# Optimization experiments

Hardware: AMD Instinct MI355X
Metric: run time of the kernel (lower is better)

Reference implementation:

```python
import jax, jax.numpy as jnp
import numpy as np

N = 1_000_000
B = 4096
L = 4
CC = 3
K = (L + 1) ** 2  # 25


def setup_inputs() -> dict:
    key = jax.random.key(0)
    ks = jax.random.split(key, 20)
    points = jax.random.normal(ks[0], (N, 3), dtype=jnp.float32)
    color = jax.random.uniform(ks[1], (N, 3), dtype=jnp.float32)
    batch = jnp.sort(jax.random.randint(ks[2], (N,), 0, B, dtype=jnp.int64))

    def lin(k, o, i, s):
        return jax.random.normal(k, (o, i), dtype=jnp.float32) * s

    inp = {
        "points": points,
        "color": color,
        "batch": batch,
        # FeatureNet 1x1 conv weights (kernel size 1 -> plain linear)
        "w1": lin(ks[3], 32, 6, 0.4), "b1": jnp.zeros((32,), jnp.float32),
        "w2": lin(ks[4], 128, 32, 0.18), "b2": jnp.zeros((128,), jnp.float32),
        "w3": lin(ks[5], 256, 128, 0.09), "b3": jnp.zeros((256,), jnp.float32),
        # FC head
        "fw1": lin(ks[6], 128, 256, 0.06), "fb1": jnp.zeros((128,), jnp.float32),
        "fw2": lin(ks[7], 64, 128, 0.09), "fb2": jnp.zeros((64,), jnp.float32),
        "fw3": lin(ks[8], K * CC, 64, 0.12), "fb3": jnp.zeros((K * CC,), jnp.float32),
        "coef_mean": jnp.zeros((K, CC), jnp.float32),
        "coef_std": jnp.ones((K, CC), jnp.float32),
    }
    return inp


def reference(points, color, batch, w1, b1, w2, b2, w3, b3,
              fw1, fb1, fw2, fb2, fw3, fb3, coef_mean, coef_std):
    # per-point shared MLP (1x1 convs == linear over channel dim)
    x = jnp.concatenate([points, color], axis=-1)          # [N, 6]
    x = jax.nn.relu(x @ w1.T + b1)                          # [N, 32]
    x = jax.nn.relu(x @ w2.T + b2)                          # [N, 128]
    x = x @ w3.T + b3                                       # [N, 256]
    # scatter_reduce(amax) onto a zeros-initialized target (include_self=True)
    # => per-segment max clamped below at 0; empty segments stay 0.
    seg = jax.ops.segment_max(x, batch, num_segments=B, indices_are_sorted=True)
    x_max = jnp.maximum(seg, 0.0)                           # [B, 256]
    # FC head
    h = jax.nn.relu(x_max @ fw1.T + fb1)                    # [B, 128]
    h = jax.nn.relu(h @ fw2.T + fb2)                        # [B, 64]
    h = h @ fw3.T + fb3                                     # [B, 75]
    out = h.reshape(-1, K, CC) * coef_std + coef_mean       # [B, 25, 3]
    return out
```

## Files before the change

kernel.cpp:

```cpp
#include <hip/hip_runtime.h>
#include <hip/hip_bf16.h>

typedef __attribute__((ext_vector_type(8))) short short8;
typedef __attribute__((ext_vector_type(16))) float f32x16;

union U8 { short8 s; unsigned int u[4]; };

static __device__ __forceinline__ unsigned short f2bf(float f) {
  unsigned int u = __float_as_uint(f);
  u += 0x7fffu + ((u >> 16) & 1u);
  return (unsigned short)(u >> 16);
}
static __device__ __forceinline__ float bf2f(unsigned short h) {
  return __uint_as_float(((unsigned int)h) << 16);
}
static __device__ __forceinline__ unsigned int cvtpk(float lo, float hi) {
  unsigned int r;
  asm("v_cvt_pk_bf16_f32 %0, %1, %2" : "=v"(r) : "v"(lo), "v"(hi));
  return r;
}
static __device__ __forceinline__ unsigned int pkrelu(float a, float b) {
  return cvtpk(fmaxf(a, 0.0f), fmaxf(b, 0.0f));
}
static __device__ __forceinline__ f32x16 MFMA(short8 a, short8 b, f32x16 c) {
  return __builtin_amdgcn_mfma_f32_32x32x16_bf16(a, b, c, 0, 0, 0);
}

__global__ void prep_weights(const float* __restrict__ w1, const float* __restrict__ w2,
                             const float* __restrict__ w3,
                             unsigned short* __restrict__ w1p, uint4* __restrict__ wimg) {
  const int i = blockIdx.x * 256 + threadIdx.x;
  if (i < 512) {
    { int c = i >> 4, k = i & 15; w1p[i] = (k < 6) ? f2bf(w1[c * 6 + k]) : (unsigned short)0; }
    const int l31 = i & 31, rest = i >> 5;
    const int g = rest & 1, n = (rest >> 1) & 1, t2 = rest >> 2;
    const float* src = w2 + (l31 + 32 * t2) * 32 + n * 16 + 8 * g;
    uint4 v;
    v.x = (unsigned)f2bf(src[0]) | ((unsigned)f2bf(src[1]) << 16);
    v.y = (unsigned)f2bf(src[2]) | ((unsigned)f2bf(src[3]) << 16);
    v.z = (unsigned)f2bf(src[4]) | ((unsigned)f2bf(src[5]) << 16);
    v.w = (unsigned)f2bf(src[6]) | ((unsigned)f2bf(src[7]) << 16);
    wimg[i] = v;
  }
  if (i < 4096) {
    const int l31 = i & 31, rest = i >> 5;
    const int g = rest & 1, k0 = (rest >> 1) & 7, t = rest >> 4;
    const float* src = w3 + (l31 + 32 * t) * 128 + k0 * 16 + 8 * g;
    uint4 v;
    v.x = (unsigned)f2bf(src[0]) | ((unsigned)f2bf(src[1]) << 16);
    v.y = (unsigned)f2bf(src[2]) | ((unsigned)f2bf(src[3]) << 16);
    v.z = (unsigned)f2bf(src[4]) | ((unsigned)f2bf(src[5]) << 16);
    v.w = (unsigned)f2bf(src[6]) | ((unsigned)f2bf(src[7]) << 16);
    wimg[512 + i] = v;
  }
}

__global__ void seg_starts(const int* __restrict__ batch, int* __restrict__ starts,
                           int N, int B) {
  const int i = blockIdx.x * 256 + threadIdx.x;
  if (i == 0) {
    const int b0 = batch[0];
    for (int s = 0; s <= b0; ++s) starts[s] = 0;
    const int bl = batch[N - 1];
    for (int s = bl + 1; s <= B; ++s) starts[s] = N;
  } else if (i < N) {
    const int a = batch[i - 1], b = batch[i];
    for (int s = a + 1; s <= b; ++s) starts[s] = i;
  }
}

__global__ __launch_bounds__(512, 4) void mlp_segmax_mfma(
    const float* __restrict__ points, const float* __restrict__ color,
    const int* __restrict__ batch,
    const unsigned short* __restrict__ w1p, const uint4* __restrict__ wimg,
    const float* __restrict__ b1, const float* __restrict__ b2, const float* __restrict__ b3,
    float* __restrict__ xmax, int* __restrict__ Pid, unsigned short* __restrict__ Pval,
    int useP, int N)
{
  __shared__ __align__(16) uint4 smem[4608];
  const int tid  = threadIdx.x;
  const int wv   = tid >> 6;
  const int lane = tid & 63;
  const int g    = lane >> 5;
  const int l31  = lane & 31;

  for (int i = tid; i < 4608; i += 512) smem[i] = wimg[i];
  __syncthreads();
  const char* w2c = (const char*)smem;
  const char* w3c = (const char*)(smem + 512);

  const short8 a1 = *reinterpret_cast<const short8*>(w1p + l31 * 16 + 8 * g);
  float b3v[8];
#pragma unroll
  for (int t = 0; t < 8; ++t) b3v[t] = b3[32 * t + l31];

  const int wid = blockIdx.x * 8 + wv;
  const long long wbase = (long long)wid * 256;
  const int rowbase = 4 * wid;
  int rowcnt = 0;
  int cur = -1;
  float rmax[8];
#pragma unroll
  for (int t = 0; t < 8; ++t) rmax[t] = -INFINITY;

  auto flushP = [&]() {
    if (cur < 0) return;
    if (useP && rowcnt < 4) {
      const int row = rowbase + rowcnt;
      ++rowcnt;
      if (lane == 0) Pid[row] = cur;
#pragma unroll
      for (int t = 0; t < 8; ++t) {
        float v = fmaxf(rmax[t], __shfl_xor(rmax[t], 32));
        if ((t >> 2) == g) Pval[row * 256 + 32 * t + l31] = f2bf(v);
      }
    } else {
#pragma unroll
      for (int t = 0; t < 8; ++t) {
        float v = fmaxf(rmax[t], __shfl_xor(rmax[t], 32));
        if (lane < 32 && v > 0.0f)
          atomicMax((int*)xmax + cur * 256 + 32 * t + lane, __float_as_int(v));
      }
    }
  };

  float n0 = 0, n1 = 0, n2 = 0, n3 = 0, n4 = 0, n5 = 0;
  int nseg = -2 - lane;
  if (wbase < (long long)N) {
    const int p = (int)wbase + l31;
    n0 = points[p * 3 + 0]; n1 = points[p * 3 + 1]; n2 = points[p * 3 + 2];
    n3 = color[p * 3 + 0];  n4 = color[p * 3 + 1];  n5 = color[p * 3 + 2];
    nseg = batch[p];
  }

  for (int it = 0; it < 8; ++it) {
    const long long base = wbase + (long long)it * 32;
    if (base >= (long long)N) break;

    const float c0 = n0, c1 = n1, c2 = n2, c3 = n3, c4 = n4, c5 = n5;
    const int segv = nseg;
    if (base + 32 < (long long)N && it < 7) {
      const int p = (int)base + 32 + l31;
      n0 = points[p * 3 + 0]; n1 = points[p * 3 + 1]; n2 = points[p * 3 + 2];
      n3 = color[p * 3 + 0];  n4 = color[p * 3 + 1];  n5 = color[p * 3 + 2];
      nseg = batch[p];
    }

    unsigned long long b1a = (unsigned long long)b1; asm volatile("" : "+s"(b1a));
    unsigned long long b2a = (unsigned long long)b2; asm volatile("" : "+s"(b2a));
    const float* b1l = (const float*)b1a;
    const float* b2l = (const float*)b2a;
    int z = 0; asm volatile("" : "+v"(z));

    const unsigned int zm = (g == 0) ? 0xffffffffu : 0u;
    U8 bin;
    bin.u[0] = cvtpk(c0, c1) & zm;
    bin.u[1] = cvtpk(c2, c3) & zm;
    bin.u[2] = cvtpk(c4, c5) & zm;
    bin.u[3] = 0;
    f32x16 ci;
#pragma unroll
    for (int q2 = 0; q2 < 4; ++q2) {
      const float4 bv = *reinterpret_cast<const float4*>(b1l + 8 * q2 + 4 * g);
      ci[4 * q2 + 0] = bv.x; ci[4 * q2 + 1] = bv.y; ci[4 * q2 + 2] = bv.z; ci[4 * q2 + 3] = bv.w;
    }
    f32x16 d1 = MFMA(a1, bin.s, ci);

    unsigned int W1[4][2];
#pragma unroll
    for (int q2 = 0; q2 < 4; ++q2) {
      W1[q2][0] = pkrelu(d1[4 * q2 + 0], d1[4 * q2 + 1]);
      W1[q2][1] = pkrelu(d1[4 * q2 + 2], d1[4 * q2 + 3]);
    }
    U8 h1f[2];
#pragma unroll
    for (int n = 0; n < 2; ++n) {
      unsigned int r0 = __shfl_xor(W1[2 * n + 1 - g][0], 32);
      unsigned int r1 = __shfl_xor(W1[2 * n + 1 - g][1], 32);
      h1f[n].u[0] = (g == 0) ? W1[2 * n + g][0] : r0;
      h1f[n].u[1] = (g == 0) ? W1[2 * n + g][1] : r1;
      h1f[n].u[2] = (g == 1) ? W1[2 * n + g][0] : r0;
      h1f[n].u[3] = (g == 1) ? W1[2 * n + g][1] : r1;
    }

    unsigned int own2[4][2][2], rc2[4][2][2];
#pragma unroll
    for (int t2 = 0; t2 < 4; ++t2) {
      f32x16 cc;
#pragma unroll
      for (int q2 = 0; q2 < 4; ++q2) {
        const float4 bv = *reinterpret_cast<const float4*>(b2l + 32 * t2 + 8 * q2 + 4 * g);
        cc[4 * q2 + 0] = bv.x; cc[4 * q2 + 1] = bv.y; cc[4 * q2 + 2] = bv.z; cc[4 * q2 + 3] = bv.w;
      }
      const short8 a20 = *reinterpret_cast<const short8*>(
          w2c + ((((t2 * 2 + 0) * 2 + g) * 32 + l31) << 4) + z);
      const short8 a21 = *reinterpret_cast<const short8*>(
          w2c + ((((t2 * 2 + 1) * 2 + g) * 32 + l31) << 4) + z);
      f32x16 d2 = MFMA(a20, h1f[0].s, cc);
      d2 = MFMA(a21, h1f[1].s, d2);
      unsigned int Wt[4][2];
#pragma unroll
      for (int q2 = 0; q2 < 4; ++q2) {
        Wt[q2][0] = pkrelu(d2[4 * q2 + 0], d2[4 * q2 + 1]);
        Wt[q2][1] = pkrelu(d2[4 * q2 + 2], d2[4 * q2 + 3]);
      }
#pragma unroll
      for (int m = 0; m < 2; ++m) {
        own2[t2][m][0] = Wt[2 * m + g][0];
        own2[t2][m][1] = Wt[2 * m + g][1];
        rc2[t2][m][0] = __shfl_xor(Wt[2 * m + 1 - g][0], 32);
        rc2[t2][m][1] = __shfl_xor(Wt[2 * m + 1 - g][1], 32);
      }
    }
    U8 a3[8];
#pragma unroll
    for (int k0 = 0; k0 < 8; ++k0) {
      const int t2 = k0 >> 1, m = k0 & 1;
      a3[k0].u[0] = (g == 0) ? own2[t2][m][0] : rc2[t2][m][0];
      a3[k0].u[1] = (g == 0) ? own2[t2][m][1] : rc2[t2][m][1];
      a3[k0].u[2] = (g == 1) ? own2[t2][m][0] : rc2[t2][m][0];
      a3[k0].u[3] = (g == 1) ? own2[t2][m][1] : rc2[t2][m][1];
    }

    const int segA = __builtin_amdgcn_readfirstlane(segv);
    const int segD = __shfl(segv, 31);
    const bool caseU = (segA == segD);
    if (segA != cur) {
      flushP();
#pragma unroll
      for (int t = 0; t < 8; ++t) rmax[t] = -INFINITY;
      cur = segA;
    }
    unsigned int bA = 0, bD = 0;
    bool restAny = false;
    int rowA = -1;
    if (!caseU) {
      bA = (unsigned int)__ballot(segv == segA);
      bD = (unsigned int)__ballot(segv == segD);
      restAny = ((bA | bD) != 0xffffffffu);
      if (useP && rowcnt < 4) {
        rowA = rowbase + rowcnt;
        ++rowcnt;
        if (lane == 0) Pid[rowA] = segA;
      }
    }

#pragma unroll
    for (int t = 0; t < 8; ++t) {
      f32x16 acc;
#pragma unroll
      for (int r2 = 0; r2 < 16; ++r2) acc[r2] = b3v[t];
#pragma unroll
      for (int k0 = 0; k0 < 8; ++k0) {
        const short8 bf = *reinterpret_cast<const short8*>(
            w3c + ((((t * 8 + k0) * 2 + g) * 32 + l31) << 4) + z);
        acc = MFMA(a3[k0].s, bf, acc);
      }
      if (caseU) {
        float m = acc[0];
#pragma unroll
        for (int r2 = 1; r2 < 16; ++r2) m = fmaxf(m, acc[r2]);
        rmax[t] = fmaxf(rmax[t], m);
      } else {
        float ma = -INFINITY, md = -INFINITY;
#pragma unroll
        for (int r2 = 0; r2 < 16; ++r2) {
          const int idx = (r2 & 3) + 8 * (r2 >> 2) + 4 * g;
          const unsigned int bit = 1u << idx;
          const float v = acc[r2];
          ma = fmaxf(ma, (bA & bit) ? v : -INFINITY);
          md = fmaxf(md, (bD & bit) ? v : -INFINITY);
        }
        if (restAny) {
#pragma unroll
          for (int r2 = 0; r2 < 16; ++r2) {
            const int idx = (r2 & 3) + 8 * (r2 >> 2) + 4 * g;
            const unsigned int bit = 1u << idx;
            if (!((bA | bD) & bit)) {
              const int sid = __shfl(segv, idx);
              const float v = acc[r2];
              if (sid >= 0 && v > 0.0f)
                atomicMax((int*)xmax + sid * 256 + 32 * t + l31, __float_as_int(v));
            }
          }
        }
        float va = fmaxf(rmax[t], ma);
        va = fmaxf(va, __shfl_xor(va, 32));
        if (rowA >= 0) {
          if ((t >> 2) == g) Pval[rowA * 256 + 32 * t + l31] = f2bf(va);
        } else if (lane < 32 && va > 0.0f) {
          atomicMax((int*)xmax + segA * 256 + 32 * t + lane, __float_as_int(va));
        }
        rmax[t] = md;
      }
    }
    if (!caseU) cur = segD;
  }
  flushP();
  if (useP && lane == 0) {
    for (int j = rowcnt; j < 4; ++j) Pid[rowbase + j] = -1;
  }
}

__global__ __launch_bounds__(256) void head_kernel(
    const float* __restrict__ xmax,
    const int* __restrict__ starts, const int* __restrict__ Pid,
    const unsigned short* __restrict__ Pval, int useP,
    const float* __restrict__ fw1, const float* __restrict__ fb1,
    const float* __restrict__ fw2, const float* __restrict__ fb2,
    const float* __restrict__ fw3, const float* __restrict__ fb3,
    const float* __restrict__ cmean, const float* __restrict__ cstd,
    float* __restrict__ out, int B)
{
  __shared__ __align__(16) float xm[16][260];
  __shared__ __align__(16) float h1b[16][132];
  __shared__ __align__(16) float h2b[16][68];

  const int t = threadIdx.x;
  const int bbase = blockIdx.x * 16;

  for (int i = t; i < 16 * 256; i += 256) {
    const int bi = i >> 8, k = i & 255;
    const int s = min(bbase + bi, B - 1);
    float acc = xmax[(long long)s * 256 + k];
    if (useP) {
      const int i0 = starts[s], i1 = starts[s + 1];
      if (i1 > i0) {
        const int w0 = i0 >> 8, w1 = (i1 - 1) >> 8;
        for (int w = w0; w <= w1; ++w) {
#pragma unroll
          for (int j = 0; j < 4; ++j) {
            const int row = 4 * w + j;
            if (Pid[row] == s) acc = fmaxf(acc, bf2f(Pval[row * 256 + k]));
          }
        }
      }
    }
    xm[bi][k] = fmaxf(acc, 0.0f);
  }
  __syncthreads();

  {
    const int bi = t >> 4, oi = t & 15;
    float acc[8];
#pragma unroll
    for (int u = 0; u < 8; ++u) acc[u] = fb1[oi * 8 + u];
    for (int k = 0; k < 256; k += 4) {
      const float4 xv = *reinterpret_cast<const float4*>(&xm[bi][k]);
#pragma unroll
      for (int u = 0; u < 8; ++u) {
        const float4 wv = *reinterpret_cast<const float4*>(fw1 + (oi * 8 + u) * 256 + k);
        acc[u] = fmaf(xv.x, wv.x, acc[u]);
        acc[u] = fmaf(xv.y, wv.y, acc[u]);
        acc[u] = fmaf(xv.z, wv.z, acc[u]);
        acc[u] = fmaf(xv.w, wv.w, acc[u]);
      }
    }
#pragma unroll
    for (int u = 0; u < 8; ++u) h1b[bi][oi * 8 + u] = fmaxf(acc[u], 0.0f);
  }
  __syncthreads();

  {
    const int bi = t >> 4, oi = t & 15;
    float acc[4];
#pragma unroll
    for (int u = 0; u < 4; ++u) acc[u] = fb2[oi * 4 + u];
    for (int k = 0; k < 128; k += 4) {
      const float4 xv = *reinterpret_cast<const float4*>(&h1b[bi][k]);
#pragma unroll
      for (int u = 0; u < 4; ++u) {
        const float4 wv = *reinterpret_cast<const float4*>(fw2 + (oi * 4 + u) * 128 + k);
        acc[u] = fmaf(xv.x, wv.x, acc[u]);
        acc[u] = fmaf(xv.y, wv.y, acc[u]);
        acc[u] = fmaf(xv.z, wv.z, acc[u]);
        acc[u] = fmaf(xv.w, wv.w, acc[u]);
      }
    }
#pragma unroll
    for (int u = 0; u < 4; ++u) h2b[bi][oi * 4 + u] = fmaxf(acc[u], 0.0f);
  }
  __syncthreads();

  for (int i = t; i < 16 * 75; i += 256) {
    const int bi = i / 75, o = i - bi * 75;
    float a = fb3[o];
    for (int k = 0; k < 64; k += 4) {
      const float4 xv = *reinterpret_cast<const float4*>(&h2b[bi][k]);
      const float4 wv = *reinterpret_cast<const float4*>(fw3 + o * 64 + k);
      a = fmaf(xv.x, wv.x, a);
      a = fmaf(xv.y, wv.y, a);
      a = fmaf(xv.z, wv.z, a);
      a = fmaf(xv.w, wv.w, a);
    }
    const int b = bbase + bi;
    if (b < B) out[(long long)b * 75 + o] = fmaf(a, cstd[o], cmean[o]);
  }
}

extern "C" void kernel_launch(void* const* d_in, const int* in_sizes, int n_in,
                              void* d_out, int out_size, void* d_ws, size_t ws_size,
                              hipStream_t stream) {
  const float* points = (const float*)d_in[0];
  const float* color  = (const float*)d_in[1];
  const int*   batch  = (const int*)d_in[2];
  const float* w1  = (const float*)d_in[3];
  const float* b1  = (const float*)d_in[4];
  const float* w2  = (const float*)d_in[5];
  const float* b2  = (const float*)d_in[6];
  const float* w3  = (const float*)d_in[7];
  const float* b3  = (const float*)d_in[8];
  const float* fw1 = (const float*)d_in[9];
  const float* fb1 = (const float*)d_in[10];
  const float* fw2 = (const float*)d_in[11];
  const float* fb2 = (const float*)d_in[12];
  const float* fw3 = (const float*)d_in[13];
  const float* fb3 = (const float*)d_in[14];
  const float* cmean = (const float*)d_in[15];
  const float* cstd  = (const float*)d_in[16];
  float* out = (float*)d_out;

  const int N = in_sizes[2];
  const int B = out_size / 75;

  const int nWavesReal = (N + 255) / 256;
  const int nBlocks = (nWavesReal + 7) / 8;
  const int NROWS = 4 * nBlocks * 8;

  char* ws = (char*)d_ws;
  float* xmax = (float*)ws;
  unsigned short* w1p = (unsigned short*)(ws + 4194304);
  uint4* wimg = (uint4*)(ws + 4198400);
  const size_t offStarts = 4272128;
  const size_t offPid  = (offStarts + (size_t)(B + 1) * 4 + 15) & ~(size_t)15;
  const size_t offPval = (offPid + (size_t)NROWS * 4 + 15) & ~(size_t)15;
  const size_t needed  = offPval + (size_t)NROWS * 256 * 2;
  const int useP = (ws_size >= needed) ? 1 : 0;
  int* starts = (int*)(ws + offStarts);
  int* Pid    = (int*)(ws + offPid);
  unsigned short* Pval = (unsigned short*)(ws + offPval);

  hipMemsetAsync(xmax, 0, (size_t)B * 256 * sizeof(float), stream);
  prep_weights<<<16, 256, 0, stream>>>(w1, w2, w3, w1p, wimg);
  if (useP)
    seg_starts<<<(N + 255) / 256, 256, 0, stream>>>(batch, starts, N, B);

  mlp_segmax_mfma<<<nBlocks, 512, 0, stream>>>(points, color, batch,
                                               w1p, wimg, b1, b2, b3,
                                               xmax, Pid, Pval, useP, N);

  head_kernel<<<(B + 15) / 16, 256, 0, stream>>>(xmax, starts, Pid, Pval, useP,
                                                 fw1, fb1, fw2, fb2, fw3, fb3,
                                                 cmean, cstd, out, B);
}
```

Measured before the change: 462.8 us.

## Fuse prep launches and replace atomics with direct stores for interior segments

Merges the memset, weight packing and segment-start kernels into one launch to cut launch overhead. In the main kernel, each wave now owns two partial rows, one for its first segment and one for its last. Segments fully interior to a wave are written to xmax with plain stores instead of atomicMax, since only one wave can touch them. The head kernel scans two partial rows per wave instead of four. This depends on batch being sorted, and it relies on interior segments being owned by a single wave.

```diff
diff --git a/kernel.cpp b/kernel.cpp
--- a/kernel.cpp
+++ b/kernel.cpp
@@ -26,10 +26,24 @@
   return __builtin_amdgcn_mfma_f32_32x32x16_bf16(a, b, c, 0, 0, 0);
 }
 
-__global__ void prep_weights(const float* __restrict__ w1, const float* __restrict__ w2,
-                             const float* __restrict__ w3,
-                             unsigned short* __restrict__ w1p, uint4* __restrict__ wimg) {
+__global__ void prep_all(const float* __restrict__ w1, const float* __restrict__ w2,
+                         const float* __restrict__ w3, const int* __restrict__ batch,
+                         unsigned short* __restrict__ w1p, uint4* __restrict__ wimg,
+                         float* __restrict__ xmax, int* __restrict__ starts,
+                         int useP, int N, int B) {
   const int i = blockIdx.x * 256 + threadIdx.x;
+  if (i < B * 256) xmax[i] = 0.0f;
+  if (useP) {
+    if (i == 0) {
+      const int b0 = batch[0];
+      for (int s = 0; s <= b0; ++s) starts[s] = 0;
+      const int bl = batch[N - 1];
+      for (int s = bl + 1; s <= B; ++s) starts[s] = N;
+    } else if (i < N) {
+      const int a = batch[i - 1], b = batch[i];
+      for (int s = a + 1; s <= b; ++s) starts[s] = i;
+    }
+  }
   if (i < 512) {
     { int c = i >> 4, k = i & 15; w1p[i] = (k < 6) ? f2bf(w1[c * 6 + k]) : (unsigned short)0; }
     const int l31 = i & 31, rest = i >> 5;
@@ -52,20 +66,6 @@
     v.z = (unsigned)f2bf(src[4]) | ((unsigned)f2bf(src[5]) << 16);
     v.w = (unsigned)f2bf(src[6]) | ((unsigned)f2bf(src[7]) << 16);
     wimg[512 + i] = v;
-  }
-}
-
-__global__ void seg_starts(const int* __restrict__ batch, int* __restrict__ starts,
-                           int N, int B) {
-  const int i = blockIdx.x * 256 + threadIdx.x;
-  if (i == 0) {
-    const int b0 = batch[0];
-    for (int s = 0; s <= b0; ++s) starts[s] = 0;
-    const int bl = batch[N - 1];
-    for (int s = bl + 1; s <= B; ++s) starts[s] = N;
-  } else if (i < N) {
-    const int a = batch[i - 1], b = batch[i];
-    for (int s = a + 1; s <= b; ++s) starts[s] = i;
   }
 }
 
@@ -96,8 +96,13 @@
 
   const int wid = blockIdx.x * 8 + wv;
   const long long wbase = (long long)wid * 256;
-  const int rowbase = 4 * wid;
-  int rowcnt = 0;
+  const int rowbase = 2 * wid;
+  bool used0 = false, used1 = false;
+  int firstSeg = -1, lastSeg = -1;
+  if (wbase < (long long)N) {
+    firstSeg = batch[(int)wbase];
+    lastSeg  = batch[min((int)wbase + 255, N - 1)];
+  }
   int cur = -1;
   float rmax[8];
 #pragma unroll
@@ -105,21 +110,30 @@
 
   auto flushP = [&]() {
     if (cur < 0) return;
-    if (useP && rowcnt < 4) {
-      const int row = rowbase + rowcnt;
-      ++rowcnt;
-      if (lane == 0) Pid[row] = cur;
-#pragma unroll
-      for (int t = 0; t < 8; ++t) {
-        float v = fmaxf(rmax[t], __shfl_xor(rmax[t], 32));
-        if ((t >> 2) == g) Pval[row * 256 + 32 * t + l31] = f2bf(v);
+    if (useP) {
+      int row = -1;
+      if (cur == firstSeg) { row = rowbase; used0 = true; }
+      else if (cur == lastSeg) { row = rowbase + 1; used1 = true; }
+      if (row >= 0) {
+        if (lane == 0) Pid[row] = cur;
+#pragma unroll
+        for (int t = 0; t < 8; ++t) {
+          float v = fmaxf(rmax[t], __shfl_xor(rmax[t], 32));
+          if ((t >> 2) == g) Pval[row * 256 + 32 * t + l31] = f2bf(v);
+        }
+      } else {
+#pragma unroll
+        for (int t = 0; t < 8; ++t) {
+          float v = fmaxf(rmax[t], __shfl_xor(rmax[t], 32));
+          if (lane < 32) xmax[(long long)cur * 256 + 32 * t + lane] = v;
+        }
       }
     } else {
 #pragma unroll
       for (int t = 0; t < 8; ++t) {
         float v = fmaxf(rmax[t], __shfl_xor(rmax[t], 32));
         if (lane < 32 && v > 0.0f)
-          atomicMax((int*)xmax + cur * 256 + 32 * t + lane, __float_as_int(v));
+          atomicMax((int*)xmax + (long long)cur * 256 + 32 * t + lane, __float_as_int(v));
       }
     }
   };
@@ -233,15 +247,16 @@
     }
     unsigned int bA = 0, bD = 0;
     bool restAny = false;
-    int rowA = -1;
+    int rowA = -1; bool dirA = false;
     if (!caseU) {
       bA = (unsigned int)__ballot(segv == segA);
       bD = (unsigned int)__ballot(segv == segD);
       restAny = ((bA | bD) != 0xffffffffu);
-      if (useP && rowcnt < 4) {
-        rowA = rowbase + rowcnt;
-        ++rowcnt;
-        if (lane == 0) Pid[rowA] = segA;
+      if (useP) {
+        if (segA == firstSeg) { rowA = rowbase; used0 = true; }
+        else if (segA == lastSeg) { rowA = rowbase + 1; used1 = true; }
+        else dirA = true;
+        if (rowA >= 0 && lane == 0) Pid[rowA] = segA;
       }
     }
 
@@ -280,7 +295,7 @@
               const int sid = __shfl(segv, idx);
               const float v = acc[r2];
               if (sid >= 0 && v > 0.0f)
-                atomicMax((int*)xmax + sid * 256 + 32 * t + l31, __float_as_int(v));
+                atomicMax((int*)xmax + (long long)sid * 256 + 32 * t + l31, __float_as_int(v));
             }
           }
         }
@@ -288,8 +303,10 @@
         va = fmaxf(va, __shfl_xor(va, 32));
         if (rowA >= 0) {
           if ((t >> 2) == g) Pval[rowA * 256 + 32 * t + l31] = f2bf(va);
+        } else if (dirA) {
+          if (lane < 32) xmax[(long long)segA * 256 + 32 * t + lane] = va;
         } else if (lane < 32 && va > 0.0f) {
-          atomicMax((int*)xmax + segA * 256 + 32 * t + lane, __float_as_int(va));
+          atomicMax((int*)xmax + (long long)segA * 256 + 32 * t + lane, __float_as_int(va));
         }
         rmax[t] = md;
       }
@@ -298,7 +315,8 @@
   }
   flushP();
   if (useP && lane == 0) {
-    for (int j = rowcnt; j < 4; ++j) Pid[rowbase + j] = -1;
+    if (!used0) Pid[rowbase] = -1;
+    if (!used1) Pid[rowbase + 1] = -1;
   }
 }
 
@@ -329,8 +347,8 @@
         const int w0 = i0 >> 8, w1 = (i1 - 1) >> 8;
         for (int w = w0; w <= w1; ++w) {
 #pragma unroll
-          for (int j = 0; j < 4; ++j) {
-            const int row = 4 * w + j;
+          for (int j = 0; j < 2; ++j) {
+            const int row = 2 * w + j;
             if (Pid[row] == s) acc = fmaxf(acc, bf2f(Pval[row * 256 + k]));
           }
         }
@@ -423,27 +441,24 @@
   const int N = in_sizes[2];
   const int B = out_size / 75;
 
-  const int nWavesReal = (N + 255) / 256;
-  const int nBlocks = (nWavesReal + 7) / 8;
-  const int NROWS = 4 * nBlocks * 8;
+  const int nWaves  = (N + 255) / 256;
+  const int nBlocks = (nWaves + 7) / 8;
+  const int NROWS   = 2 * nBlocks * 8;
 
   char* ws = (char*)d_ws;
-  float* xmax = (float*)ws;
-  unsigned short* w1p = (unsigned short*)(ws + 4194304);
-  uint4* wimg = (uint4*)(ws + 4198400);
-  const size_t offStarts = 4272128;
-  const size_t offPid  = (offStarts + (size_t)(B + 1) * 4 + 15) & ~(size_t)15;
-  const size_t offPval = (offPid + (size_t)NROWS * 4 + 15) & ~(size_t)15;
-  const size_t needed  = offPval + (size_t)NROWS * 256 * 2;
+  size_t off = 0;
+  float* xmax = (float*)(ws + off);            off += (size_t)B * 256 * 4;
+  unsigned short* w1p = (unsigned short*)(ws + off); off += 1024;
+  uint4* wimg = (uint4*)(ws + off);            off += 4608 * 16;
+  int* starts = (int*)(ws + off);              off += ((size_t)(B + 1) * 4 + 15) & ~(size_t)15;
+  int* Pid = (int*)(ws + off);                 off += ((size_t)NROWS * 4 + 15) & ~(size_t)15;
+  unsigned short* Pval = (unsigned short*)(ws + off);
+  const size_t needed = off + (size_t)NROWS * 512;
   const int useP = (ws_size >= needed) ? 1 : 0;
-  int* starts = (int*)(ws + offStarts);
-  int* Pid    = (int*)(ws + offPid);
-  unsigned short* Pval = (unsigned short*)(ws + offPval);
-
-  hipMemsetAsync(xmax, 0, (size_t)B * 256 * sizeof(float), stream);
-  prep_weights<<<16, 256, 0, stream>>>(w1, w2, w3, w1p, wimg);
-  if (useP)
-    seg_starts<<<(N + 255) / 256, 256, 0, stream>>>(batch, starts, N, B);
+
+  const int M = (N > B * 256) ? N : B * 256;
+  prep_all<<<(M + 255) / 256, 256, 0, stream>>>(w1, w2, w3, batch, w1p, wimg,
+                                                xmax, starts, useP, N, B);
 
   mlp_segmax_mfma<<<nBlocks, 512, 0, stream>>>(points, color, batch,
                                                w1p, wimg, b1, b2, b3,
```

After: 492.5 us. +6.4%, slower.
